# Performance work log

Hardware: AMD Instinct MI355X
Metric: run time of the kernel (lower is better)

Reference implementation:

```python
import jax, jax.numpy as jnp
import numpy as np

N_NODES = 50000


def _gcn_conv(x, edge_index, W, b):
    # PyG GCNConv (default flags): add self-loops, symmetric normalization,
    # linear transform, scatter-add aggregation, bias.
    N = x.shape[0]
    row, col = edge_index[0], edge_index[1]  # messages flow row -> col
    loop = jnp.arange(N)
    row_f = jnp.concatenate([row, loop])
    col_f = jnp.concatenate([col, loop])
    deg = jax.ops.segment_sum(jnp.ones(col_f.shape[0], dtype=x.dtype), col_f,
                              num_segments=N)
    deg_inv_sqrt = jnp.where(deg > 0, jax.lax.rsqrt(jnp.maximum(deg, 1e-12)), 0.0)
    norm = deg_inv_sqrt[row_f] * deg_inv_sqrt[col_f]  # [E+N]
    h = x @ W                                          # [N, out]
    msg = h[row_f] * norm[:, None]                     # gather + scale
    out = jax.ops.segment_sum(msg, col_f, num_segments=N)  # scatter-add
    return out + b


def setup_inputs() -> dict:
    key = jax.random.key(0)
    ks = jax.random.split(key, 6)
    d_in, d_hid, d_out = 128, 128, 64
    E = 800000
    x = jax.random.normal(ks[0], (N_NODES, d_in), dtype=jnp.float32)
    edge_index = jax.random.randint(ks[1], (2, E), 0, N_NODES, dtype=jnp.int64)
    edge_label = jax.random.uniform(ks[2], (100000,), dtype=jnp.float32)
    edge_label_index = jax.random.randint(ks[3], (2, 100000), 0, N_NODES,
                                          dtype=jnp.int64)
    # Glorot-style init for GCNConv linear weights
    W1 = jax.random.normal(ks[4], (d_in, d_hid), dtype=jnp.float32) / np.sqrt(d_in)
    b1 = jnp.zeros((d_hid,), dtype=jnp.float32)
    W2 = jax.random.normal(ks[5], (d_hid, d_out), dtype=jnp.float32) / np.sqrt(d_hid)
    b2 = jnp.zeros((d_out,), dtype=jnp.float32)
    return {"x": x, "edge_index": edge_index, "edge_label": edge_label,
            "edge_label_index": edge_label_index,
            "W1": W1, "b1": b1, "W2": W2, "b2": b2}


def reference(x, edge_index, edge_label, edge_label_index, W1, b1, W2, b2):
    h = jax.nn.relu(_gcn_conv(x, edge_index, W1, b1))
    # dropout is identity in eval mode (training=False)
    z = _gcn_conv(h, edge_index, W2, b2)
    return z
```

## Files before the change

kernel.cpp:

```cpp
#include <hip/hip_runtime.h>


typedef unsigned int u32;
typedef unsigned short ushort;
typedef __attribute__((ext_vector_type(8))) short short8;
typedef __attribute__((ext_vector_type(4))) float floatx4;

static inline int cdiv_l(long a, int b) { return (int)((a + b - 1) / b); }

constexpr int NPB  = 512;
constexpr int EPB  = 4096;
constexpr int MAXB = 128;
constexpr int CAP  = 12288;

__device__ __forceinline__ u32 pack_bf16(float a, float b) {
  union { float f; u32 i; } ua, ub;
  ua.f = a; ub.f = b;
  u32 x = (ua.i + 0x7fffu + ((ua.i >> 16) & 1u)) >> 16;
  u32 y = (ub.i + 0x7fffu + ((ub.i >> 16) & 1u)) & 0xffff0000u;
  return x | y;
}

__device__ __forceinline__ short bf16r(float f) {
  union { float f; u32 i; } u; u.f = f;
  return (short)((u.i + 0x7fffu + ((u.i >> 16) & 1u)) >> 16);
}

__device__ __forceinline__ void dq8(float* a, uint2 v, float sd) {
  a[0] += (float)(v.x & 255u) * sd;
  a[1] += (float)((v.x >> 8) & 255u) * sd;
  a[2] += (float)((v.x >> 16) & 255u) * sd;
  a[3] += (float)(v.x >> 24) * sd;
  a[4] += (float)(v.y & 255u) * sd;
  a[5] += (float)((v.y >> 8) & 255u) * sd;
  a[6] += (float)((v.y >> 16) & 255u) * sd;
  a[7] += (float)(v.y >> 24) * sd;
}

template <int W>
__device__ __forceinline__ int lane_sort(int v, int l) {
#pragma unroll
  for (int k = 2; k <= W; k <<= 1) {
#pragma unroll
    for (int j = k >> 1; j > 0; j >>= 1) {
      int o = __shfl_xor(v, j, W);
      bool asc = ((l & k) == 0);
      bool low = ((l & j) == 0);
      v = (asc == low) ? min(v, o) : max(v, o);
    }
  }
  return v;
}

__global__ __launch_bounds__(256) void k_pack(
    const float* __restrict__ W1, const float* __restrict__ W2,
    u32* __restrict__ w1f, u32* __restrict__ w2f, int* __restrict__ cur) {
  const int tid = threadIdx.x;
  const int b = blockIdx.x;
  if (b == 0 && tid < MAXB) cur[tid] = 0;
  if (b < 8) {
    const int s = b * 256 + tid;
    const int lane = s & 63, frag = s >> 6;
    const int kc = frag >> 3, cb = frag & 7;
    const float* src =
        W1 + (long)(kc * 32 + (lane >> 4) * 8) * 128 + cb * 16 + (lane & 15);
    u32 o[4];
#pragma unroll
    for (int p = 0; p < 4; ++p)
      o[p] = pack_bf16(src[(2 * p) * 128], src[(2 * p + 1) * 128]);
    *(uint4*)(w1f + (long)s * 4) = make_uint4(o[0], o[1], o[2], o[3]);
  } else {
    const int s = (b - 8) * 256 + tid;
    const int lane = s & 63, frag = s >> 6;
    const int kc = frag >> 2, cb = frag & 3;
    const float* src =
        W2 + (long)(kc * 32 + (lane >> 4) * 8) * 64 + cb * 16 + (lane & 15);
    u32 o[4];
#pragma unroll
    for (int p = 0; p < 4; ++p)
      o[p] = pack_bf16(src[(2 * p) * 64], src[(2 * p + 1) * 64]);
    *(uint4*)(w2f + (long)s * 4) = make_uint4(o[0], o[1], o[2], o[3]);
  }
}

__global__ __launch_bounds__(256) void k_fused1(
    const int* __restrict__ ei, int* __restrict__ cur, u32* __restrict__ ebuf,
    int E, int NBE,
    const float* __restrict__ x, const u32* __restrict__ w1f,
    u32* __restrict__ h8, float* __restrict__ scale, int N) {
  __shared__ float eb[4][16 * 133];
  const int tid = threadIdx.x;

  if (blockIdx.x < (unsigned)NBE) {
    u32* ecache = (u32*)&eb[0][0];
    int* hist   = (int*)&eb[2][0];
    int* curs   = hist + MAXB;
    const int* ecol = ei + E;
    if (tid < MAXB) hist[tid] = 0;
    __syncthreads();
    const int base = blockIdx.x * EPB;
#pragma unroll
    for (int j = 0; j < EPB / 256; ++j) {
      int e = base + j * 256 + tid;
      u32 pk = 0xffffffffu;
      if (e < E) {
        u32 r = (u32)ei[e];
        u32 c = (u32)ecol[e];
        pk = r | (c << 16);
        atomicAdd(hist + (c >> 9), 1);
      }
      ecache[j * 256 + tid] = pk;
    }
    __syncthreads();
    if (tid < MAXB) {
      int n = hist[tid];
      curs[tid] = tid * CAP + (n ? atomicAdd(cur + tid, n) : 0);
    }
    __syncthreads();
#pragma unroll
    for (int j = 0; j < EPB / 256; ++j) {
      u32 pk = ecache[j * 256 + tid];
      if (pk != 0xffffffffu) {
        u32 c = pk >> 16;
        int b = c >> 9;
        int p = atomicAdd(curs + b, 1);
        if (p < (b + 1) * CAP)
          ebuf[p] = (pk & 0xffffu) | ((c & (NPB - 1)) << 16);
      }
    }
    return;
  }

  constexpr int K = 128, NC = 8, LROW = 133;
  const int w = tid >> 6, lane = tid & 63;
  const int quad = lane >> 4, n16 = lane & 15;
  const int row0 = ((blockIdx.x - NBE) * 4 + w) * 16;

  floatx4 acc[NC];
#pragma unroll
  for (int c = 0; c < NC; ++c) acc[c] = {0.f, 0.f, 0.f, 0.f};

  const int am = row0 + n16;
  const bool av = am < N;
  const float* arow = x + (long)am * K;
  const short8* wf = (const short8*)w1f;

#pragma unroll
  for (int kc = 0; kc < 4; ++kc) {
    const int kb = kc * 32 + quad * 8;
    float4 a0 = make_float4(0.f, 0.f, 0.f, 0.f);
    float4 a1 = make_float4(0.f, 0.f, 0.f, 0.f);
    if (av) {
      a0 = *(const float4*)(arow + kb);
      a1 = *(const float4*)(arow + kb + 4);
    }
    short8 af;
    af[0] = bf16r(a0.x); af[1] = bf16r(a0.y); af[2] = bf16r(a0.z); af[3] = bf16r(a0.w);
    af[4] = bf16r(a1.x); af[5] = bf16r(a1.y); af[6] = bf16r(a1.z); af[7] = bf16r(a1.w);
#pragma unroll
    for (int c = 0; c < NC; ++c) {
      short8 bf = wf[(kc * 8 + c) * 64 + lane];
      acc[c] = __builtin_amdgcn_mfma_f32_16x16x32_bf16(af, bf, acc[c], 0, 0, 0);
    }
  }

  float* ep = eb[w];
#pragma unroll
  for (int c = 0; c < NC; ++c)
#pragma unroll
    for (int r = 0; r < 4; ++r)
      ep[(quad * 4 + r) * LROW + c * 16 + n16] = acc[c][r];
  __syncthreads();

  const int rr = lane >> 2, seg = lane & 3;
  const float* rowp = ep + rr * LROW + seg * 32;
  float m = 0.f;
#pragma unroll
  for (int c = 0; c < 32; ++c) m = fmaxf(m, fabsf(rowp[c]));
  m = fmaxf(m, __shfl_xor(m, 1, 4));
  m = fmaxf(m, __shfl_xor(m, 2, 4));
  const float inv = (m > 0.f) ? 127.f / m : 0.f;
  const float s = m / 127.f;
  u32 q[8];
#pragma unroll
  for (int wd = 0; wd < 8; ++wd) {
    u32 b0 = (u32)((int)rintf(rowp[wd * 4 + 0] * inv) + 128);
    u32 b1 = (u32)((int)rintf(rowp[wd * 4 + 1] * inv) + 128);
    u32 b2 = (u32)((int)rintf(rowp[wd * 4 + 2] * inv) + 128);
    u32 b3 = (u32)((int)rintf(rowp[wd * 4 + 3] * inv) + 128);
    q[wd] = (b0 & 255u) | ((b1 & 255u) << 8) | ((b2 & 255u) << 16) | (b3 << 24);
  }
  const int rg = row0 + rr;
  if (rg < N) {
    uint4* dst = (uint4*)(h8 + (long)rg * 32 + seg * 8);
    dst[0] = make_uint4(q[0], q[1], q[2], q[3]);
    dst[1] = make_uint4(q[4], q[5], q[6], q[7]);
    if (seg == 0) scale[rg] = s;
  }
}

__global__ __launch_bounds__(NPB) void k_csr(const u32* __restrict__ ebuf,
                                             const int* __restrict__ cur,
                                             const float* __restrict__ scale,
                                             int* __restrict__ off,
                                             int* __restrict__ deg,
                                             float* __restrict__ dis,
                                             float* __restrict__ sd,
                                             ushort* __restrict__ csr, int N) {
  __shared__ int cnt[NPB];
  __shared__ int curl[NPB];
  __shared__ int wsum[NPB / 64];
  const int tid = threadIdx.x;
  const int b = blockIdx.x;
  const int s = b * CAP;
  const int e = s + min(cur[b], CAP);
  cnt[tid] = 0;
  __syncthreads();
  for (int i = s + tid; i < e; i += NPB)
    atomicAdd(cnt + (ebuf[i] >> 16), 1);
  __syncthreads();
  const int lane = tid & 63, w = tid >> 6;
  int v = cnt[tid];
  int incl = v;
#pragma unroll
  for (int d = 1; d < 64; d <<= 1) {
    int x = __shfl_up(incl, d, 64);
    if (lane >= d) incl += x;
  }
  if (lane == 63) wsum[w] = incl;
  __syncthreads();
  if (w == 0 && lane < NPB / 64) {
    int sv = wsum[lane];
#pragma unroll
    for (int d = 1; d < NPB / 64; d <<= 1) {
      int x = __shfl_up(sv, d, 64);
      if (lane >= d) sv += x;
    }
    wsum[lane] = sv;
  }
  __syncthreads();
  int excl = ((w > 0) ? wsum[w - 1] : 0) + incl - v;
  int node = b * NPB + tid;
  if (node < N) {
    float dv = rsqrtf((float)v + 1.0f);
    off[node] = s + excl;
    deg[node] = v;
    dis[node] = dv;
    sd[node] = scale[node] * dv;
  }
  curl[tid] = excl;
  __syncthreads();
  for (int i = s + tid; i < e; i += NPB) {
    u32 pk = ebuf[i];
    int p = atomicAdd(curl + (pk >> 16), 1);
    csr[s + p] = (ushort)(pk & 0xffffu);
  }
}

__global__ __launch_bounds__(256) void k_gg(
    const uint2* __restrict__ h8, const int* __restrict__ off,
    const int* __restrict__ deg, const ushort* __restrict__ csr,
    const float* __restrict__ dis, const float* __restrict__ sd,
    const float* __restrict__ b1, const u32* __restrict__ w2f,
    u32* __restrict__ h2, float* __restrict__ s2, int N) {
  constexpr int LG = 65;
  constexpr int LC = 66;
  __shared__ u32 lg[16 * LG];
  __shared__ float cb[16 * LC];
  const int tid = threadIdx.x;
  const int r = tid >> 4;
  const int lf = tid & 15;
  const int row0 = blockIdx.x * 16;
  const int n = row0 + r;

  u32 gw[4] = {0, 0, 0, 0};
  if (n < N) {
    const int s = off[n], e = s + deg[n];
    const float dn = dis[n];
    float acc[8] = {};
    float K = 0.f;
    {
      float sn = sd[n];
      dq8(acc, h8[(long)n * 16 + lf], sn);
      K += sn;
    }
    for (int j = s; j < e; j += 16) {
      int idx = j + lf;
      int cs = (idx < e) ? (int)csr[idx] : 0x7fffffff;
      cs = lane_sort<16>(cs, lf);
      const int cnt = min(e - j, 16);
      int t = 0;
      for (; t + 4 <= cnt; t += 4) {
        int s0 = __shfl(cs, t, 16);
        int s1 = __shfl(cs, t + 1, 16);
        int s2_ = __shfl(cs, t + 2, 16);
        int s3 = __shfl(cs, t + 3, 16);
        float d0 = sd[s0], d1 = sd[s1], d2 = sd[s2_], d3 = sd[s3];
        uint2 v0 = h8[(long)s0 * 16 + lf];
        uint2 v1 = h8[(long)s1 * 16 + lf];
        uint2 v2 = h8[(long)s2_ * 16 + lf];
        uint2 v3 = h8[(long)s3 * 16 + lf];
        dq8(acc, v0, d0); dq8(acc, v1, d1); dq8(acc, v2, d2); dq8(acc, v3, d3);
        K += (d0 + d1) + (d2 + d3);
      }
      for (; t < cnt; ++t) {
        int s0 = __shfl(cs, t, 16);
        float d0 = sd[s0];
        dq8(acc, h8[(long)s0 * 16 + lf], d0);
        K += d0;
      }
    }
    const int f8 = lf * 8;
    const float4 bv0 = *(const float4*)(b1 + f8);
    const float4 bv1 = *(const float4*)(b1 + f8 + 4);
    const float bb[8] = {bv0.x, bv0.y, bv0.z, bv0.w, bv1.x, bv1.y, bv1.z, bv1.w};
    const float kc = 128.f * K;
#pragma unroll
    for (int q = 0; q < 8; ++q)
      acc[q] = fmaxf((acc[q] - kc) * dn + bb[q], 0.f);
#pragma unroll
    for (int q = 0; q < 4; ++q)
      gw[q] = pack_bf16(acc[2 * q], acc[2 * q + 1]);
  }
#pragma unroll
  for (int q = 0; q < 4; ++q) lg[r * LG + lf * 4 + q] = gw[q];
  __syncthreads();

  const int w = tid >> 6, lane = tid & 63;
  const int quad = lane >> 4, n16 = lane & 15;
  floatx4 acc4 = {0.f, 0.f, 0.f, 0.f};
#pragma unroll
  for (int kc = 0; kc < 4; ++kc) {
    const int kb = kc * 32 + quad * 8;
    const u32* ap = &lg[n16 * LG + (kb >> 1)];
    u32 aw[4] = {ap[0], ap[1], ap[2], ap[3]};
    short8 af = *(short8*)aw;
    short8 bf = ((const short8*)w2f)[(kc * 4 + w) * 64 + lane];
    acc4 = __builtin_amdgcn_mfma_f32_16x16x32_bf16(af, bf, acc4, 0, 0, 0);
  }
  float dd[4];
#pragma unroll
  for (int r4 = 0; r4 < 4; ++r4) {
    int rg = row0 + quad * 4 + r4;
    dd[r4] = (rg < N) ? dis[rg] : 0.f;
  }
#pragma unroll
  for (int r4 = 0; r4 < 4; ++r4)
    cb[(quad * 4 + r4) * LC + w * 16 + n16] = acc4[r4] * dd[r4];
  __syncthreads();

  const int rr2 = tid >> 4, lf2 = tid & 15;
  const float* rp = cb + rr2 * LC + lf2 * 4;
  float mx = fmaxf(fmaxf(fabsf(rp[0]), fabsf(rp[1])),
                   fmaxf(fabsf(rp[2]), fabsf(rp[3])));
  mx = fmaxf(mx, __shfl_xor(mx, 1, 16));
  mx = fmaxf(mx, __shfl_xor(mx, 2, 16));
  mx = fmaxf(mx, __shfl_xor(mx, 4, 16));
  mx = fmaxf(mx, __shfl_xor(mx, 8, 16));
  const float inv2 = (mx > 0.f) ? 127.f / mx : 0.f;
  const int rg2 = row0 + rr2;
  if (rg2 < N) {
    u32 q0 = (u32)((int)rintf(rp[0] * inv2) + 128);
    u32 q1 = (u32)((int)rintf(rp[1] * inv2) + 128);
    u32 q2 = (u32)((int)rintf(rp[2] * inv2) + 128);
    u32 q3 = (u32)((int)rintf(rp[3] * inv2) + 128);
    h2[(long)rg2 * 16 + lf2] =
        (q0 & 255u) | ((q1 & 255u) << 8) | ((q2 & 255u) << 16) | (q3 << 24);
    if (lf2 == 0) s2[rg2] = mx / 127.f;
  }
}

__global__ __launch_bounds__(256) void k_gather2(
    const uint2* __restrict__ hs, const int* __restrict__ off,
    const int* __restrict__ deg, const ushort* __restrict__ csr,
    const float* __restrict__ dis, const float* __restrict__ sc2,
    const float* __restrict__ bias, float* __restrict__ out, int N) {
  constexpr int L = 8;
  const int local = threadIdx.x / L;
  const int lf = threadIdx.x % L;
  const int n = blockIdx.x * (256 / L) + local;
  if (n >= N) return;
  const int s = off[n], e = s + deg[n];
  float acc[8] = {};
  float K = 0.f;
  {
    float t0 = sc2[n];
    dq8(acc, hs[(long)n * L + lf], t0);
    K += t0;
  }
  for (int j = s; j < e; j += 8) {
    int idx = j + lf;
    int cs = (idx < e) ? (int)csr[idx] : 0x7fffffff;
    cs = lane_sort<8>(cs, lf);
    const int cnt = min(e - j, 8);
    int t = 0;
    for (; t + 4 <= cnt; t += 4) {
      int s0 = __shfl(cs, t, 8);
      int s1 = __shfl(cs, t + 1, 8);
      int s2_ = __shfl(cs, t + 2, 8);
      int s3 = __shfl(cs, t + 3, 8);
      float d0 = sc2[s0], d1 = sc2[s1], d2 = sc2[s2_], d3 = sc2[s3];
      uint2 v0 = hs[(long)s0 * L + lf];
      uint2 v1 = hs[(long)s1 * L + lf];
      uint2 v2 = hs[(long)s2_ * L + lf];
      uint2 v3 = hs[(long)s3 * L + lf];
      dq8(acc, v0, d0); dq8(acc, v1, d1); dq8(acc, v2, d2); dq8(acc, v3, d3);
      K += (d0 + d1) + (d2 + d3);
    }
    for (; t < cnt; ++t) {
      int s0 = __shfl(cs, t, 8);
      float d0 = sc2[s0];
      dq8(acc, hs[(long)s0 * L + lf], d0);
      K += d0;
    }
  }
  const float d = dis[n];
  const float kc = 128.f * K;
  const int f8 = lf * 8;
  const float4 b0 = *(const float4*)(bias + f8);
  const float4 b1v = *(const float4*)(bias + f8 + 4);
  float4 o0, o1;
  o0.x = (acc[0] - kc) * d + b0.x;
  o0.y = (acc[1] - kc) * d + b0.y;
  o0.z = (acc[2] - kc) * d + b0.z;
  o0.w = (acc[3] - kc) * d + b0.w;
  o1.x = (acc[4] - kc) * d + b1v.x;
  o1.y = (acc[5] - kc) * d + b1v.y;
  o1.z = (acc[6] - kc) * d + b1v.z;
  o1.w = (acc[7] - kc) * d + b1v.w;
  *(float4*)(out + (long)n * 64 + f8) = o0;
  *(float4*)(out + (long)n * 64 + f8 + 4) = o1;
}

extern "C" void kernel_launch(void* const* d_in, const int* in_sizes, int n_in,
                              void* d_out, int out_size, void* d_ws, size_t ws_size,
                              hipStream_t stream) {
  const float* x  = (const float*)d_in[0];
  const int*   ei = (const int*)d_in[1];
  const float* W1 = (const float*)d_in[4];
  const float* b1 = (const float*)d_in[5];
  const float* W2 = (const float*)d_in[6];
  const float* b2 = (const float*)d_in[7];
  float* out = (float*)d_out;

  const int N = in_sizes[0] / 128;
  const int E = in_sizes[1] / 2;
  const int NBKT = cdiv_l(N, NPB);
  const int NBE  = cdiv_l(E, EPB);
  const int G1   = cdiv_l(N, 64);

  const long Np = (N + 64) & ~63L;
  const long BW = (long)NBKT * CAP;
  int*    cur   = (int*)d_ws;
  int*    off   = cur + 128;
  int*    deg   = off + Np;
  float*  dis   = (float*)(deg + Np);
  float*  scale = dis + Np;
  float*  sd    = scale + Np;
  float*  s2    = sd + Np;
  u32*    w1f   = (u32*)(s2 + Np);
  u32*    w2f   = w1f + 8192;
  u32*    ebuf  = w2f + 4096;
  ushort* csr   = (ushort*)(ebuf + BW);
  u32*    h8    = (u32*)(csr + BW);
  u32*    h2    = h8 + (long)N * 32;

  k_pack<<<12, 256, 0, stream>>>(W1, W2, w1f, w2f, cur);

  k_fused1<<<NBE + G1, 256, 0, stream>>>(ei, cur, ebuf, E, NBE, x, w1f, h8,
                                         scale, N);

  k_csr<<<NBKT, NPB, 0, stream>>>(ebuf, cur, scale, off, deg, dis, sd, csr, N);

  k_gg<<<cdiv_l(N, 16), 256, 0, stream>>>((const uint2*)h8, off, deg, csr,
                                          dis, sd, b1, w2f, h2, s2, N);

  k_gather2<<<cdiv_l(N, 32), 256, 0, stream>>>((const uint2*)h2, off, deg, csr,
                                               dis, s2, b2, out, N);
}
```

Before: 158.8 us.

## Pad CSR segments to 8 and load neighbor indices as 16-byte vectors

The CSR build pads each node's segment start to a multiple of 8 entries, so every segment offset is 16-byte aligned. Both gather kernels then read 8 neighbor indices per 16-byte vector load, broadcast to all lanes. This replaces the per-lane index load, the bitonic lane sort and the shuffle broadcasts, and unrolls the gather to 8 rows per step. It drops the sorted access order that may have helped cache locality, and the padding spends more of each block's fixed CSR capacity.

After: 152.1 us. 4.2% less time.

```diff
diff --git a/kernel.cpp b/kernel.cpp
--- a/kernel.cpp
+++ b/kernel.cpp
@@ -4,6 +4,7 @@
 typedef unsigned int u32;
 typedef unsigned short ushort;
 typedef __attribute__((ext_vector_type(8))) short short8;
+typedef __attribute__((ext_vector_type(8))) unsigned short us8;
 typedef __attribute__((ext_vector_type(4))) float floatx4;
 
 static inline int cdiv_l(long a, int b) { return (int)((a + b - 1) / b); }
@@ -35,21 +36,6 @@
   a[5] += (float)((v.y >> 8) & 255u) * sd;
   a[6] += (float)((v.y >> 16) & 255u) * sd;
   a[7] += (float)(v.y >> 24) * sd;
-}
-
-template <int W>
-__device__ __forceinline__ int lane_sort(int v, int l) {
-#pragma unroll
-  for (int k = 2; k <= W; k <<= 1) {
-#pragma unroll
-    for (int j = k >> 1; j > 0; j >>= 1) {
-      int o = __shfl_xor(v, j, W);
-      bool asc = ((l & k) == 0);
-      bool low = ((l & j) == 0);
-      v = (asc == low) ? min(v, o) : max(v, o);
-    }
-  }
-  return v;
 }
 
 __global__ __launch_bounds__(256) void k_pack(
@@ -220,8 +206,9 @@
     atomicAdd(cnt + (ebuf[i] >> 16), 1);
   __syncthreads();
   const int lane = tid & 63, w = tid >> 6;
-  int v = cnt[tid];
-  int incl = v;
+  const int v = cnt[tid];
+  const int vp = (v + 7) & ~7;
+  int incl = vp;
 #pragma unroll
   for (int d = 1; d < 64; d <<= 1) {
     int x = __shfl_up(incl, d, 64);
@@ -239,7 +226,7 @@
     wsum[lane] = sv;
   }
   __syncthreads();
-  int excl = ((w > 0) ? wsum[w - 1] : 0) + incl - v;
+  int excl = ((w > 0) ? wsum[w - 1] : 0) + incl - vp;
   int node = b * NPB + tid;
   if (node < N) {
     float dv = rsqrtf((float)v + 1.0f);
@@ -284,30 +271,35 @@
       dq8(acc, h8[(long)n * 16 + lf], sn);
       K += sn;
     }
-    for (int j = s; j < e; j += 16) {
-      int idx = j + lf;
-      int cs = (idx < e) ? (int)csr[idx] : 0x7fffffff;
-      cs = lane_sort<16>(cs, lf);
-      const int cnt = min(e - j, 16);
-      int t = 0;
-      for (; t + 4 <= cnt; t += 4) {
-        int s0 = __shfl(cs, t, 16);
-        int s1 = __shfl(cs, t + 1, 16);
-        int s2_ = __shfl(cs, t + 2, 16);
-        int s3 = __shfl(cs, t + 3, 16);
-        float d0 = sd[s0], d1 = sd[s1], d2 = sd[s2_], d3 = sd[s3];
-        uint2 v0 = h8[(long)s0 * 16 + lf];
-        uint2 v1 = h8[(long)s1 * 16 + lf];
-        uint2 v2 = h8[(long)s2_ * 16 + lf];
-        uint2 v3 = h8[(long)s3 * 16 + lf];
-        dq8(acc, v0, d0); dq8(acc, v1, d1); dq8(acc, v2, d2); dq8(acc, v3, d3);
-        K += (d0 + d1) + (d2 + d3);
-      }
-      for (; t < cnt; ++t) {
-        int s0 = __shfl(cs, t, 16);
-        float d0 = sd[s0];
-        dq8(acc, h8[(long)s0 * 16 + lf], d0);
-        K += d0;
+    int j = s;
+    for (; j + 8 <= e; j += 8) {
+      us8 ev = *(const us8*)(csr + j);
+      const int i0 = ev[0], i1 = ev[1], i2 = ev[2], i3 = ev[3];
+      const int i4 = ev[4], i5 = ev[5], i6 = ev[6], i7 = ev[7];
+      const float d0 = sd[i0], d1 = sd[i1], d2 = sd[i2], d3 = sd[i3];
+      const float d4 = sd[i4], d5 = sd[i5], d6 = sd[i6], d7 = sd[i7];
+      uint2 v0 = h8[(long)i0 * 16 + lf];
+      uint2 v1 = h8[(long)i1 * 16 + lf];
+      uint2 v2 = h8[(long)i2 * 16 + lf];
+      uint2 v3 = h8[(long)i3 * 16 + lf];
+      uint2 v4 = h8[(long)i4 * 16 + lf];
+      uint2 v5 = h8[(long)i5 * 16 + lf];
+      uint2 v6 = h8[(long)i6 * 16 + lf];
+      uint2 v7 = h8[(long)i7 * 16 + lf];
+      dq8(acc, v0, d0); dq8(acc, v1, d1); dq8(acc, v2, d2); dq8(acc, v3, d3);
+      dq8(acc, v4, d4); dq8(acc, v5, d5); dq8(acc, v6, d6); dq8(acc, v7, d7);
+      K += ((d0 + d1) + (d2 + d3)) + ((d4 + d5) + (d6 + d7));
+    }
+    if (j < e) {
+      us8 ev = *(const us8*)(csr + j);
+#pragma unroll
+      for (int t = 0; t < 8; ++t) {
+        if (j + t < e) {
+          const int it = ev[t];
+          const float dt = sd[it];
+          dq8(acc, h8[(long)it * 16 + lf], dt);
+          K += dt;
+        }
       }
     }
     const int f8 = lf * 8;
@@ -388,30 +380,35 @@
     dq8(acc, hs[(long)n * L + lf], t0);
     K += t0;
   }
-  for (int j = s; j < e; j += 8) {
-    int idx = j + lf;
-    int cs = (idx < e) ? (int)csr[idx] : 0x7fffffff;
-    cs = lane_sort<8>(cs, lf);
-    const int cnt = min(e - j, 8);
-    int t = 0;
-    for (; t + 4 <= cnt; t += 4) {
-      int s0 = __shfl(cs, t, 8);
-      int s1 = __shfl(cs, t + 1, 8);
-      int s2_ = __shfl(cs, t + 2, 8);
-      int s3 = __shfl(cs, t + 3, 8);
-      float d0 = sc2[s0], d1 = sc2[s1], d2 = sc2[s2_], d3 = sc2[s3];
-      uint2 v0 = hs[(long)s0 * L + lf];
-      uint2 v1 = hs[(long)s1 * L + lf];
-      uint2 v2 = hs[(long)s2_ * L + lf];
-      uint2 v3 = hs[(long)s3 * L + lf];
-      dq8(acc, v0, d0); dq8(acc, v1, d1); dq8(acc, v2, d2); dq8(acc, v3, d3);
-      K += (d0 + d1) + (d2 + d3);
-    }
-    for (; t < cnt; ++t) {
-      int s0 = __shfl(cs, t, 8);
-      float d0 = sc2[s0];
-      dq8(acc, hs[(long)s0 * L + lf], d0);
-      K += d0;
+  int j = s;
+  for (; j + 8 <= e; j += 8) {
+    us8 ev = *(const us8*)(csr + j);
+    const int i0 = ev[0], i1 = ev[1], i2 = ev[2], i3 = ev[3];
+    const int i4 = ev[4], i5 = ev[5], i6 = ev[6], i7 = ev[7];
+    const float d0 = sc2[i0], d1 = sc2[i1], d2 = sc2[i2], d3 = sc2[i3];
+    const float d4 = sc2[i4], d5 = sc2[i5], d6 = sc2[i6], d7 = sc2[i7];
+    uint2 v0 = hs[(long)i0 * L + lf];
+    uint2 v1 = hs[(long)i1 * L + lf];
+    uint2 v2 = hs[(long)i2 * L + lf];
+    uint2 v3 = hs[(long)i3 * L + lf];
+    uint2 v4 = hs[(long)i4 * L + lf];
+    uint2 v5 = hs[(long)i5 * L + lf];
+    uint2 v6 = hs[(long)i6 * L + lf];
+    uint2 v7 = hs[(long)i7 * L + lf];
+    dq8(acc, v0, d0); dq8(acc, v1, d1); dq8(acc, v2, d2); dq8(acc, v3, d3);
+    dq8(acc, v4, d4); dq8(acc, v5, d5); dq8(acc, v6, d6); dq8(acc, v7, d7);
+    K += ((d0 + d1) + (d2 + d3)) + ((d4 + d5) + (d6 + d7));
+  }
+  if (j < e) {
+    us8 ev = *(const us8*)(csr + j);
+#pragma unroll
+    for (int t = 0; t < 8; ++t) {
+      if (j + t < e) {
+        const int it = ev[t];
+        const float dt = sc2[it];
+        dq8(acc, hs[(long)it * L + lf], dt);
+        K += dt;
+      }
     }
   }
   const float d = dis[n];
```
